# Kernel optimization log

Hardware: AMD Instinct MI355X
Metric: run time of the kernel (lower is better)

Reference implementation:

```python
import jax, jax.numpy as jnp
import numpy as np

H = 12  # num_heads

def _attn(q, k, v):
    sim = jnp.einsum('bid,bjd->bij', q, k)
    a = jax.nn.softmax(sim, axis=-1)
    return jnp.einsum('bij,bjd->bid', a, v)

def _layernorm(x, g, b, eps=1e-5):
    mu = x.mean(-1, keepdims=True)
    var = ((x - mu) ** 2).mean(-1, keepdims=True)
    return (x - mu) * jax.lax.rsqrt(var + eps) * g + b

def setup_inputs() -> dict:
    key = jax.random.key(0)
    ks = jax.random.split(key, 8)
    B, F, NP, D, DT, NT = 8, 8, 196, 768, 512, 77
    N = 1 + F * NP
    s = 0.02
    return {
        'x': jax.random.normal(ks[0], (B, N, D), jnp.float32),
        'y': jax.random.normal(ks[1], (B, NT, DT), jnp.float32),
        'y_mask': jnp.zeros((B, NT), jnp.float32),
        'f': F,
        'w_qkv': jax.random.normal(ks[2], (D, 3 * D), jnp.float32) * s,
        'w_proj': jax.random.normal(ks[3], (D, D), jnp.float32) * s,
        'b_proj': jnp.zeros((D,), jnp.float32),
        'w_kv_text': jax.random.normal(ks[4], (DT, 2 * D), jnp.float32) * s,
        'w_q_i2t': jax.random.normal(ks[5], (D, D), jnp.float32) * s,
        'w_proj_i2t': jax.random.normal(ks[6], (D, D), jnp.float32) * s,
        'b_proj_i2t': jnp.zeros((D,), jnp.float32),
        'alpha_i2t': jnp.full((1,), 0.1, jnp.float32),
        'ln_g': jnp.ones((D,), jnp.float32),
        'ln_b': jnp.zeros((D,), jnp.float32),
    }

def reference(x, y, y_mask, f, w_qkv, w_proj, b_proj, w_kv_text, w_q_i2t,
              w_proj_i2t, b_proj_i2t, alpha_i2t, ln_g, ln_b):
    B, N, D = x.shape
    d = D // H
    scale = d ** -0.5
    qkv = x @ w_qkv  # [B, N, 3D]
    q, k, v = jnp.split(qkv, 3, axis=-1)
    to_bh = lambda t: t.reshape(B, N, H, d).transpose(0, 2, 1, 3).reshape(B * H, N, d)
    q, k, v = map(to_bh, (q, k, v))
    q = q * scale
    cls_q, q_ = q[:, :1], q[:, 1:]
    cls_k, k_ = k[:, :1], k[:, 1:]
    cls_v, v_ = v[:, :1], v[:, 1:]
    # cls token attends to everything
    cls_out = _attn(cls_q, k, v)  # [B*H, 1, d]
    # divided space attention: 'b (f n) d -> (b f) n d'
    n = (N - 1) // f
    split_f = lambda t: t.reshape(B * H * f, n, d)
    q_, k_, v_ = map(split_f, (q_, k_, v_))
    rep = lambda t: jnp.broadcast_to(t[:, None], (B * H, f, 1, d)).reshape(B * H * f, 1, d)
    k_ = jnp.concatenate([rep(cls_k), k_], axis=1)  # [B*H*f, n+1, d]
    v_ = jnp.concatenate([rep(cls_v), v_], axis=1)
    out = _attn(q_, k_, v_).reshape(B * H, N - 1, d)
    out = jnp.concatenate([cls_out, out], axis=1)  # [B*H, N, d]
    out = out.reshape(B, H, N, d).transpose(0, 2, 1, 3).reshape(B, N, D)
    x_out = out @ w_proj + b_proj
    # image-to-text cross attention
    NT = y.shape[1]
    kv = (y @ w_kv_text).reshape(B, NT, 2, H, d).transpose(2, 0, 3, 1, 4)
    k_t, v_t = kv[0], kv[1]  # [B, H, NT, d]
    q_i = (_layernorm(x_out, ln_g, ln_b) @ w_q_i2t).reshape(B, N, H, d).transpose(0, 2, 1, 3)
    q_i = q_i * (d ** -0.5)
    a = jnp.einsum('bhnd,bhmd->bhnm', q_i, k_t) + y_mask[:, None, None, :]
    a = jax.nn.softmax(a, axis=-1)
    yo = jnp.einsum('bhnm,bhmd->bhnd', a, v_t).transpose(0, 2, 1, 3).reshape(B, N, D)
    yo = yo @ w_proj_i2t + b_proj_i2t
    return x_out + alpha_i2t * yo
```

## Files before the change

kernel.cpp:

```cpp
#include <hip/hip_runtime.h>

typedef __bf16 bf16x8 __attribute__((ext_vector_type(8)));
typedef float f32x4 __attribute__((ext_vector_type(4)));
typedef unsigned short us_t;

#define DEV __device__ __forceinline__

DEV float bf2f(unsigned short u) {
  union { unsigned int i; float f; } c; c.i = ((unsigned int)u) << 16; return c.f;
}
DEV unsigned short f2bf(float f) {
  union { float f; unsigned int i; } c; c.f = f;
  return (unsigned short)((c.i + 0x7FFFu + ((c.i >> 16) & 1u)) >> 16);
}
DEV unsigned int cvt_pk_bf16(float lo, float hi) {
  unsigned int r;
  asm("v_cvt_pk_bf16_f32 %0, %1, %2" : "=v"(r) : "v"(lo), "v"(hi));
  return r;
}

union FragU { bf16x8 v; unsigned short u[8]; };

DEV void gld_lds16(const void* g, void* l) {
  __builtin_amdgcn_global_load_lds((const __attribute__((address_space(1))) void*)g,
                                   (__attribute__((address_space(3))) void*)l, 16, 0, 0);
}

#define MFMA(a, b, c) __builtin_amdgcn_mfma_f32_16x16x32_bf16((a), (b), (c), 0, 0, 0)

#define BB 8
#define NN 1569
#define DD 768
#define HH 12
#define DH 64
#define FF 8
#define NFR 196
#define NTT 77
#define DT_ 512
#define MROWS 12552
#define MTEXT 616

__global__ void cvt_fused(const float* __restrict__ xin, unsigned short* __restrict__ xout, int n4x,
                          const float* __restrict__ yin, unsigned short* __restrict__ yout, int n4y) {
  int i = blockIdx.x * blockDim.x + threadIdx.x;
  int stride = gridDim.x * blockDim.x;
  int total = n4x + n4y;
  for (; i < total; i += stride) {
    const float4* src; ushort4* dst; int idx;
    if (i < n4x) { src = (const float4*)xin; dst = (ushort4*)xout; idx = i; }
    else         { src = (const float4*)yin; dst = (ushort4*)yout; idx = i - n4x; }
    float4 v = src[idx];
    ushort4 o;
    o.x = f2bf(v.x); o.y = f2bf(v.y); o.z = f2bf(v.z); o.w = f2bf(v.w);
    dst[idx] = o;
  }
}

struct TJobs {
  const float* in[5];
  unsigned short* out[5];
  int R[5], C[5];
};

__global__ __launch_bounds__(256) void transpose_all(TJobs j) {
  __shared__ float tile[32][33];
  int z = blockIdx.z;
  int R = j.R[z], C = j.C[z];
  int bx = blockIdx.x * 32;
  int by = blockIdx.y * 32;
  if (bx >= C || by >= R) return;
  const float* in = j.in[z];
  unsigned short* out = j.out[z];
  int tx = threadIdx.x & 31;
  int ty0 = threadIdx.x >> 5;
  for (int dy = 0; dy < 32; dy += 8) {
    int r = by + ty0 + dy, c = bx + tx;
    tile[ty0 + dy][tx] = (r < R && c < C) ? in[(size_t)r * C + c] : 0.f;
  }
  __syncthreads();
  for (int dy = 0; dy < 32; dy += 8) {
    int orow = bx + ty0 + dy;
    int ocol = by + tx;
    if (orow < C && ocol < R) out[(size_t)orow * R + ocol] = f2bf(tile[tx][ty0 + dy]);
  }
}

enum { EPI_QKV = 0, EPI_XOUT = 1, EPI_QI = 2, EPI_KVT = 3, EPI_FINAL = 4 };

struct EpiParams {
  float* outf;
  unsigned short *o0, *o1, *o2;
  const float *bias, *aux, *alphap;
};

template <int EPI>
__global__ __launch_bounds__(256)
void gemm_bt(const unsigned short* __restrict__ A, const unsigned short* __restrict__ Bt,
             int M, int K, EpiParams ep) {
  __shared__ __align__(16) unsigned short lA[3][128 * 32];
  __shared__ __align__(16) unsigned short lB[3][128 * 32];
  const int nbx = gridDim.x, nwg = gridDim.x * gridDim.y;
  int flat = blockIdx.y * nbx + blockIdx.x;
  {
    int q = nwg >> 3, r = nwg & 7;
    int xcd = flat & 7, i = flat >> 3;
    flat = (xcd < r ? xcd * (q + 1) : r * (q + 1) + (xcd - r) * q) + i;
  }
  const int brow = (flat / nbx) * 128, bcol = (flat % nbx) * 128;
  const int t = threadIdx.x, wave = t >> 6, lane = t & 63, g = lane >> 4, l15 = lane & 15;
  const int wr = wave >> 1, wc = wave & 1;

  int dsto[2];
  const unsigned short *pA[2], *pB[2];
#pragma unroll
  for (int c = 0; c < 2; ++c) {
    int sb = wave * 1024 + c * 512;
    int slot = sb + lane * 8;
    int row = slot >> 5;
    int gl = (slot >> 3) & 3;
    int swz = gl ^ ((row >> 1) & 3);
    int ra = brow + row; if (ra > M - 1) ra = M - 1;
    dsto[c] = sb;
    pA[c] = A + (size_t)ra * K + swz * 8;
    pB[c] = Bt + (size_t)(bcol + row) * K + swz * 8;
  }

#define STG(s, k0) do { \
    gld_lds16(pA[0] + (k0), &lA[s][dsto[0]]); \
    gld_lds16(pB[0] + (k0), &lB[s][dsto[0]]); \
    gld_lds16(pA[1] + (k0), &lA[s][dsto[1]]); \
    gld_lds16(pB[1] + (k0), &lB[s][dsto[1]]); \
    __builtin_amdgcn_sched_barrier(0); } while (0)

  f32x4 acc[4][4];
#pragma unroll
  for (int i = 0; i < 4; ++i)
#pragma unroll
    for (int j = 0; j < 4; ++j) acc[i][j] = {0.f, 0.f, 0.f, 0.f};

  const int nk = K >> 5;
  STG(0, 0);
  if (nk > 1) STG(1, 32);

  for (int kt = 0; kt < nk; ++kt) {
    const int s = kt % 3;
    if (kt + 2 < nk) STG((kt + 2) % 3, (kt + 2) << 5);
    if (kt + 2 < nk)      { asm volatile("s_waitcnt vmcnt(8)" ::: "memory"); }
    else if (kt + 1 < nk) { asm volatile("s_waitcnt vmcnt(4)" ::: "memory"); }
    else                  { asm volatile("s_waitcnt vmcnt(0)" ::: "memory"); }
    __builtin_amdgcn_sched_barrier(0);
    asm volatile("s_barrier" ::: "memory");
    __builtin_amdgcn_sched_barrier(0);

    FragU af[4], bf[4];
#pragma unroll
    for (int i = 0; i < 4; ++i) {
      int rowa = wr * 64 + i * 16 + l15;
      int swa = g ^ ((rowa >> 1) & 3);
      af[i].v = *(const bf16x8*)(&lA[s][rowa * 32 + swa * 8]);
      int rowb = wc * 64 + i * 16 + l15;
      int swb = g ^ ((rowb >> 1) & 3);
      bf[i].v = *(const bf16x8*)(&lB[s][rowb * 32 + swb * 8]);
    }
#pragma unroll
    for (int i = 0; i < 4; ++i)
#pragma unroll
      for (int j = 0; j < 4; ++j)
        acc[i][j] = MFMA(af[i].v, bf[j].v, acc[i][j]);

    asm volatile("s_waitcnt lgkmcnt(0)" ::: "memory");
    __builtin_amdgcn_sched_barrier(0);
    asm volatile("s_barrier" ::: "memory");
    __builtin_amdgcn_sched_barrier(0);
  }
#undef STG

#pragma unroll
  for (int i = 0; i < 4; ++i) {
#pragma unroll
    for (int r = 0; r < 4; ++r) {
      int mrow = brow + wr * 64 + i * 16 + g * 4 + r;
      if (mrow >= M) continue;
      int bidx = 0, nn = 0, tt = 0;
      if constexpr (EPI == EPI_QKV || EPI == EPI_QI) { bidx = mrow / NN; nn = mrow - bidx * NN; }
      if constexpr (EPI == EPI_KVT) { bidx = mrow / NTT; tt = mrow - bidx * NTT; }
#pragma unroll
      for (int j = 0; j < 4; ++j) {
        int col = bcol + wc * 64 + j * 16 + l15;
        float val = acc[i][j][r];
        if constexpr (EPI == EPI_XOUT) {
          ep.outf[(size_t)mrow * DD + col] = val + ep.bias[col];
        } else if constexpr (EPI == EPI_FINAL) {
          size_t o = (size_t)mrow * DD + col;
          ep.outf[o] = ep.aux[o] + ep.alphap[0] * (val + ep.bias[col]);
        } else if constexpr (EPI == EPI_QKV) {
          int which = col / DD; int within = col - which * DD;
          int h = within >> 6, dd2 = within & 63;
          size_t dstp = (((size_t)bidx * HH + h) * NN + nn) * DH + dd2;
          if (which == 0) ep.o0[dstp] = f2bf(val * 0.125f);
          else if (which == 1) ep.o1[dstp] = f2bf(val);
          else ep.o2[dstp] = f2bf(val);
        } else if constexpr (EPI == EPI_QI) {
          int h = col >> 6, dd2 = col & 63;
          ep.o0[(((size_t)bidx * HH + h) * NN + nn) * DH + dd2] = f2bf(val * 0.125f);
        } else if constexpr (EPI == EPI_KVT) {
          int kvi = col / DD; int within = col - kvi * DD;
          int h = within >> 6, dd2 = within & 63;
          size_t dstp = (((size_t)bidx * HH + h) * NTT + tt) * DH + dd2;
          if (kvi == 0) ep.o0[dstp] = f2bf(val);
          else ep.o1[dstp] = f2bf(val);
        }
      }
    }
  }
}

__global__ __launch_bounds__(256)
void attn_all(const unsigned short* __restrict__ qg, const unsigned short* __restrict__ kg,
              const unsigned short* __restrict__ vg, unsigned short* __restrict__ outg) {
  __shared__ __align__(16) char smem[224 * 64 * 2 + 64 * 232 * 2];
  const int t = threadIdx.x, lane = t & 63, g = lane >> 4, l15 = lane & 15;
  const int wave = t >> 6;

  if (blockIdx.x < 768) {
    unsigned short* lK = (unsigned short*)smem;
    unsigned short* lV = (unsigned short*)(smem + 224 * 64 * 2);
    const int bid = blockIdx.x, bh = bid >> 3, fi = bid & 7;
    const int b = bh / HH, h = bh - b * HH;
    const size_t base = (size_t)bh * NN * DH;

#pragma unroll
    for (int c = 0; c < 7; ++c) {
      int gI = t + 256 * c;
      int elem = gI * 8, row = elem >> 6, gl = (elem >> 3) & 7;
      int srcg = gl ^ (row & 7);
      int rr = row < 197 ? row : 196;
      int nrow = (rr == 0) ? 0 : (fi * NFR + rr);
      gld_lds16(kg + base + (size_t)nrow * DH + srcg * 8, &lK[elem]);
    }
    {
      float4 vreg[7]; int vkey[7], ve[7];
#pragma unroll
      for (int c = 0; c < 7; ++c) {
        int gI = t + 256 * c;
        if (gI < 1576) {
          int key = gI >> 3, e = gI & 7;
          int nrow = (key == 0) ? 0 : (fi * NFR + key);
          vreg[c] = *(const float4*)(vg + base + (size_t)nrow * DH + e * 8);
          vkey[c] = key; ve[c] = e;
        }
      }
#pragma unroll
      for (int c = 0; c < 7; ++c) {
        int gI = t + 256 * c;
        if (gI < 1576) {
          const unsigned short* u = (const unsigned short*)&vreg[c];
          int d0 = ve[c] * 8, key = vkey[c];
#pragma unroll
          for (int z = 0; z < 8; ++z) lV[(d0 + z) * 232 + key] = u[z];
        }
      }
      for (int idx = t; idx < 27 * 64; idx += 256) {
        int key = 197 + (idx >> 6), dd = idx & 63;
        lV[dd * 232 + key] = 0;
      }
    }
    __syncthreads();

    for (int qt = wave; qt < 13; qt += 4) {
      int qr = qt * 16 + l15; if (qr > 195) qr = 195;
      const unsigned short* qp = qg + base + (size_t)(1 + fi * NFR + qr) * DH + g * 8;
      bf16x8 bq0 = *(const bf16x8*)(qp);
      bf16x8 bq1 = *(const bf16x8*)(qp + 32);
      f32x4 s[13];
#pragma unroll
      for (int kt2 = 0; kt2 < 13; ++kt2) {
        int krow = kt2 * 16 + l15;
        int rb = krow * 64;
        int sw0 = (g ^ (krow & 7)) * 8;
        int sw1 = ((4 + g) ^ (krow & 7)) * 8;
        f32x4 a = {0.f, 0.f, 0.f, 0.f};
        a = MFMA(*(const bf16x8*)(&lK[rb + sw0]), bq0, a);
        a = MFMA(*(const bf16x8*)(&lK[rb + sw1]), bq1, a);
        s[kt2] = a;
      }
      float m = -1e30f;
#pragma unroll
      for (int kt2 = 0; kt2 < 13; ++kt2)
#pragma unroll
        for (int r = 0; r < 4; ++r) {
          int key = kt2 * 16 + g * 4 + r;
          if (key >= 197) s[kt2][r] = -1e30f;
          m = fmaxf(m, s[kt2][r]);
        }
      m = fmaxf(m, __shfl_xor(m, 16));
      m = fmaxf(m, __shfl_xor(m, 32));
      float sum = 0.f;
#pragma unroll
      for (int kt2 = 0; kt2 < 13; ++kt2)
#pragma unroll
        for (int r = 0; r < 4; ++r) { float p = __expf(s[kt2][r] - m); s[kt2][r] = p; sum += p; }
      sum += __shfl_xor(sum, 16);
      sum += __shfl_xor(sum, 32);
      float inv = 1.f / sum;
#pragma unroll
      for (int kt2 = 0; kt2 < 13; ++kt2)
#pragma unroll
        for (int r = 0; r < 4; ++r) s[kt2][r] *= inv;
      unsigned int pk2[13][2];
#pragma unroll
      for (int c2 = 0; c2 < 13; ++c2) {
        pk2[c2][0] = cvt_pk_bf16(s[c2][0], s[c2][1]);
        pk2[c2][1] = cvt_pk_bf16(s[c2][2], s[c2][3]);
      }
      f32x4 o[4];
#pragma unroll
      for (int dt = 0; dt < 4; ++dt) o[dt] = {0.f, 0.f, 0.f, 0.f};
#pragma unroll
      for (int K32 = 0; K32 < 7; ++K32) {
        FragU af;
        unsigned int* aw = (unsigned int*)&af;
#pragma unroll
        for (int w = 0; w < 4; ++w) {
          int srcl = l15 + 16 * ((((lane >> 4) & 1) * 8 + 2 * w) >> 2);
          int v0 = __shfl((int)pk2[2 * K32][w & 1], srcl, 64);
          int v1 = (2 * K32 + 1 < 13) ? __shfl((int)pk2[2 * K32 + 1][w & 1], srcl, 64) : 0;
          aw[w] = (unsigned int)((g < 2) ? v0 : v1);
        }
#pragma unroll
        for (int dt = 0; dt < 4; ++dt) {
          const bf16x8 bv = *(const bf16x8*)(&lV[(dt * 16 + l15) * 232 + K32 * 32 + g * 8]);
          o[dt] = MFMA(af.v, bv, o[dt]);
        }
      }
#pragma unroll
      for (int dt = 0; dt < 4; ++dt)
#pragma unroll
        for (int r = 0; r < 4; ++r) {
          int qrow = qt * 16 + g * 4 + r;
          if (qrow < 196) {
            size_t nrow = 1 + (size_t)fi * NFR + qrow;
            outg[((size_t)b * NN + nrow) * DD + h * DH + dt * 16 + l15] = f2bf(o[dt][r]);
          }
        }
    }
  } else {
    float* q0 = (float*)smem;
    float* sc = (float*)(smem + 256);
    float* red = (float*)(smem + 256 + NN * 4);
    float* opart2 = (float*)(smem + 256 + NN * 4 + 1024);
    const int bh = blockIdx.x - 768, b = bh / HH, h = bh - b * HH;
    const size_t base = (size_t)bh * NN * DH;
    if (t < 64) q0[t] = bf2f(qg[base + t]);
    __syncthreads();
    for (int j = t; j < NN; j += 256) {
      const unsigned short* kr = kg + base + (size_t)j * DH;
      float s = 0.f;
#pragma unroll
      for (int dd = 0; dd < 64; dd += 8) {
        float4 raw = *(const float4*)(kr + dd);
        const unsigned short* pu = (const unsigned short*)&raw;
#pragma unroll
        for (int z = 0; z < 8; ++z) s += q0[dd + z] * bf2f(pu[z]);
      }
      sc[j] = s;
    }
    __syncthreads();
    float lm = -1e30f;
    for (int j = t; j < NN; j += 256) lm = fmaxf(lm, sc[j]);
    red[t] = lm; __syncthreads();
    for (int off = 128; off > 0; off >>= 1) { if (t < off) red[t] = fmaxf(red[t], red[t + off]); __syncthreads(); }
    float m = red[0];
    __syncthreads();
    float ls = 0.f;
    for (int j = t; j < NN; j += 256) { float p = __expf(sc[j] - m); sc[j] = p; ls += p; }
    __syncthreads();
    red[t] = ls; __syncthreads();
    for (int off = 128; off > 0; off >>= 1) { if (t < off) red[t] += red[t + off]; __syncthreads(); }
    float invS = 1.f / red[0];
    int jg = t >> 3, db = t & 7;
    float o8[8];
#pragma unroll
    for (int z = 0; z < 8; ++z) o8[z] = 0.f;
    for (int j = jg; j < NN; j += 32) {
      float sj = sc[j];
      float4 raw = *(const float4*)(vg + base + (size_t)j * DH + db * 8);
      const unsigned short* pu = (const unsigned short*)&raw;
#pragma unroll
      for (int z = 0; z < 8; ++z) o8[z] += sj * bf2f(pu[z]);
    }
#pragma unroll
    for (int z = 0; z < 8; ++z) opart2[jg * 66 + db * 8 + z] = o8[z];
    __syncthreads();
    if (t < 64) {
      float r = 0.f;
      for (int p2 = 0; p2 < 32; ++p2) r += opart2[p2 * 66 + t];
      outg[((size_t)b * NN) * DD + h * DH + t] = f2bf(r * invS);
    }
  }
}

__global__ __launch_bounds__(256)
void i2t_attn(const unsigned short* __restrict__ qg, const unsigned short* __restrict__ ktg,
              const unsigned short* __restrict__ vtg, const float* __restrict__ mask,
              unsigned short* __restrict__ outg) {
  __shared__ __align__(16) unsigned short lK[80 * 64];
  __shared__ __align__(16) unsigned short lV[64 * 104];
  const int bid = blockIdx.x;
  const int bh = bid % 96, chunk = bid / 96;
  const int b = bh / HH, h = bh - b * HH;
  const int t = threadIdx.x, wave = t >> 6, lane = t & 63, g = lane >> 4, l15 = lane & 15;
  const size_t kvbase = (size_t)bh * NTT * DH;
#pragma unroll
  for (int c = 0; c < 3; ++c) {
    int gI = t + 256 * c;
    if (gI < 640) {
      int elem = gI * 8, row = elem >> 6, gl = (elem >> 3) & 7;
      int srcg = gl ^ (row & 7);
      int rr = row < NTT ? row : NTT - 1;
      gld_lds16(ktg + kvbase + (size_t)rr * DH + srcg * 8, &lK[elem]);
    }
  }
  {
    float4 vreg[3]; int vkey[3], ve[3];
#pragma unroll
    for (int c = 0; c < 3; ++c) {
      int gI = t + 256 * c;
      if (gI < 616) {
        int key = gI >> 3, e = gI & 7;
        vreg[c] = *(const float4*)(vtg + kvbase + (size_t)key * DH + e * 8);
        vkey[c] = key; ve[c] = e;
      }
    }
#pragma unroll
    for (int c = 0; c < 3; ++c) {
      int gI = t + 256 * c;
      if (gI < 616) {
        const unsigned short* u = (const unsigned short*)&vreg[c];
        int d0 = ve[c] * 8, key = vkey[c];
#pragma unroll
        for (int z = 0; z < 8; ++z) lV[(d0 + z) * 104 + key] = u[z];
      }
    }
    for (int idx = t; idx < 27 * 64; idx += 256) {
      int key = NTT + (idx >> 6), dd = idx & 63;
      lV[dd * 104 + key] = 0;
    }
  }
  __syncthreads();
  const size_t qbase = (size_t)bh * NN * DH;
#pragma unroll
  for (int i4 = 0; i4 < 4; ++i4) {
    int qt = chunk * 16 + i4 * 4 + wave;
    if (qt >= 99) continue;
    int qr = qt * 16 + l15; if (qr > NN - 1) qr = NN - 1;
    const unsigned short* qp = qg + qbase + (size_t)qr * DH + g * 8;
    bf16x8 bq0 = *(const bf16x8*)(qp);
    bf16x8 bq1 = *(const bf16x8*)(qp + 32);
    f32x4 s[5];
#pragma unroll
    for (int kt2 = 0; kt2 < 5; ++kt2) {
      int krow = kt2 * 16 + l15;
      int rb = krow * 64;
      int sw0 = (g ^ (krow & 7)) * 8;
      int sw1 = ((4 + g) ^ (krow & 7)) * 8;
      f32x4 a = {0.f, 0.f, 0.f, 0.f};
      a = MFMA(*(const bf16x8*)(&lK[rb + sw0]), bq0, a);
      a = MFMA(*(const bf16x8*)(&lK[rb + sw1]), bq1, a);
      s[kt2] = a;
    }
    float m = -1e30f;
#pragma unroll
    for (int kt2 = 0; kt2 < 5; ++kt2)
#pragma unroll
      for (int r = 0; r < 4; ++r) {
        int key = kt2 * 16 + g * 4 + r;
        if (key < NTT) s[kt2][r] += mask[b * NTT + key];
        else s[kt2][r] = -1e30f;
        m = fmaxf(m, s[kt2][r]);
      }
    m = fmaxf(m, __shfl_xor(m, 16));
    m = fmaxf(m, __shfl_xor(m, 32));
    float sum = 0.f;
#pragma unroll
    for (int kt2 = 0; kt2 < 5; ++kt2)
#pragma unroll
      for (int r = 0; r < 4; ++r) { float p = __expf(s[kt2][r] - m); s[kt2][r] = p; sum += p; }
    sum += __shfl_xor(sum, 16);
    sum += __shfl_xor(sum, 32);
    float inv = 1.f / sum;
#pragma unroll
    for (int kt2 = 0; kt2 < 5; ++kt2)
#pragma unroll
      for (int r = 0; r < 4; ++r) s[kt2][r] *= inv;
    unsigned int pk2[5][2];
#pragma unroll
    for (int c2 = 0; c2 < 5; ++c2) {
      pk2[c2][0] = cvt_pk_bf16(s[c2][0], s[c2][1]);
      pk2[c2][1] = cvt_pk_bf16(s[c2][2], s[c2][3]);
    }
    f32x4 o[4];
#pragma unroll
    for (int dt = 0; dt < 4; ++dt) o[dt] = {0.f, 0.f, 0.f, 0.f};
#pragma unroll
    for (int K32 = 0; K32 < 3; ++K32) {
      FragU af;
      unsigned int* aw = (unsigned int*)&af;
#pragma unroll
      for (int w = 0; w < 4; ++w) {
        int srcl = l15 + 16 * ((((lane >> 4) & 1) * 8 + 2 * w) >> 2);
        int v0 = __shfl((int)pk2[2 * K32][w & 1], srcl, 64);
        int v1 = (2 * K32 + 1 < 5) ? __shfl((int)pk2[2 * K32 + 1][w & 1], srcl, 64) : 0;
        aw[w] = (unsigned int)((g < 2) ? v0 : v1);
      }
#pragma unroll
      for (int dt = 0; dt < 4; ++dt) {
        const bf16x8 bv = *(const bf16x8*)(&lV[(dt * 16 + l15) * 104 + K32 * 32 + g * 8]);
        o[dt] = MFMA(af.v, bv, o[dt]);
      }
    }
#pragma unroll
    for (int dt = 0; dt < 4; ++dt)
#pragma unroll
      for (int r = 0; r < 4; ++r) {
        int qrow = qt * 16 + g * 4 + r;
        if (qrow < NN)
          outg[((size_t)b * NN + qrow) * DD + h * DH + dt * 16 + l15] = f2bf(o[dt][r]);
      }
  }
}

__global__ __launch_bounds__(256)
void ln_kernel(const float* __restrict__ x, const float* __restrict__ gam,
               const float* __restrict__ bet, unsigned short* __restrict__ out) {
  __shared__ float red[256];
  const int row = blockIdx.x, t = threadIdx.x;
  const size_t base = (size_t)row * DD;
  float v0 = x[base + t], v1 = x[base + t + 256], v2 = x[base + t + 512];
  red[t] = v0 + v1 + v2; __syncthreads();
  for (int off = 128; off > 0; off >>= 1) { if (t < off) red[t] += red[t + off]; __syncthreads(); }
  float mu = red[0] * (1.f / 768.f);
  __syncthreads();
  float d0 = v0 - mu, d1 = v1 - mu, d2 = v2 - mu;
  red[t] = d0 * d0 + d1 * d1 + d2 * d2; __syncthreads();
  for (int off = 128; off > 0; off >>= 1) { if (t < off) red[t] += red[t + off]; __syncthreads(); }
  float rs = rsqrtf(red[0] * (1.f / 768.f) + 1e-5f);
  out[base + t] = f2bf(d0 * rs * gam[t] + bet[t]);
  out[base + t + 256] = f2bf(d1 * rs * gam[t + 256] + bet[t + 256]);
  out[base + t + 512] = f2bf(d2 * rs * gam[t + 512] + bet[t + 512]);
}

static constexpr size_t SZ_WQKVT = (size_t)2304 * 768 * 2;
static constexpr size_t SZ_W768  = (size_t)768 * 768 * 2;
static constexpr size_t SZ_WKVT  = (size_t)1536 * 512 * 2;
static constexpr size_t SZ_XB    = (size_t)MROWS * DD * 2;
static constexpr size_t SZ_YB    = (size_t)MTEXT * DT_ * 2;
static constexpr size_t SZ_KT    = (size_t)96 * NTT * DH * 2;

static constexpr size_t OFF_WQKVT = 0;
static constexpr size_t OFF_WPROJT = OFF_WQKVT + SZ_WQKVT;
static constexpr size_t OFF_WKVT = OFF_WPROJT + SZ_W768;
static constexpr size_t OFF_WQIT = OFF_WKVT + SZ_WKVT;
static constexpr size_t OFF_WPIT = OFF_WQIT + SZ_W768;
static constexpr size_t OFF_XB  = OFF_WPIT + SZ_W768;
static constexpr size_t OFF_YB  = OFF_XB + SZ_XB;
static constexpr size_t OFF_QB  = OFF_YB + SZ_YB;
static constexpr size_t OFF_KB  = OFF_QB + SZ_XB;
static constexpr size_t OFF_VB  = OFF_KB + SZ_XB;
static constexpr size_t OFF_XOUT = OFF_VB + SZ_XB;

extern "C" void kernel_launch(void* const* d_in, const int* in_sizes, int n_in,
                              void* d_out, int out_size, void* d_ws, size_t ws_size,
                              hipStream_t stream) {
  const float* x      = (const float*)d_in[0];
  const float* y      = (const float*)d_in[1];
  const float* y_mask = (const float*)d_in[2];
  const float* w_qkv  = (const float*)d_in[4];
  const float* w_proj = (const float*)d_in[5];
  const float* b_proj = (const float*)d_in[6];
  const float* w_kv   = (const float*)d_in[7];
  const float* w_qi   = (const float*)d_in[8];
  const float* w_pi   = (const float*)d_in[9];
  const float* b_pi   = (const float*)d_in[10];
  const float* alpha  = (const float*)d_in[11];
  const float* ln_g   = (const float*)d_in[12];
  const float* ln_b   = (const float*)d_in[13];
  float* out = (float*)d_out;
  char* ws = (char*)d_ws;

  us_t* wqkvT = (us_t*)(ws + OFF_WQKVT);
  us_t* wprojT = (us_t*)(ws + OFF_WPROJT);
  us_t* wkvT = (us_t*)(ws + OFF_WKVT);
  us_t* wqiT = (us_t*)(ws + OFF_WQIT);
  us_t* wpiT = (us_t*)(ws + OFF_WPIT);
  us_t* xb  = (us_t*)(ws + OFF_XB);
  us_t* yb  = (us_t*)(ws + OFF_YB);
  us_t* qb  = (us_t*)(ws + OFF_QB);
  us_t* kb  = (us_t*)(ws + OFF_KB);
  us_t* vb  = (us_t*)(ws + OFF_VB);
  float* xoutf = (float*)(ws + OFF_XOUT);
  us_t* attn_out = xb;
  us_t* lnout = qb;
  us_t* qib = kb;
  us_t* ktb = vb;
  us_t* vtb = (us_t*)(ws + OFF_VB + SZ_KT);
  us_t* i2t_out = xb;

  cvt_fused<<<2048, 256, 0, stream>>>(x, xb, MROWS * DD / 4, y, yb, MTEXT * DT_ / 4);
  TJobs tj;
  tj.in[0] = w_qkv;  tj.out[0] = wqkvT;  tj.R[0] = 768; tj.C[0] = 2304;
  tj.in[1] = w_proj; tj.out[1] = wprojT; tj.R[1] = 768; tj.C[1] = 768;
  tj.in[2] = w_kv;   tj.out[2] = wkvT;   tj.R[2] = 512; tj.C[2] = 1536;
  tj.in[3] = w_qi;   tj.out[3] = wqiT;   tj.R[3] = 768; tj.C[3] = 768;
  tj.in[4] = w_pi;   tj.out[4] = wpiT;   tj.R[4] = 768; tj.C[4] = 768;
  transpose_all<<<dim3(72, 24, 5), 256, 0, stream>>>(tj);

  EpiParams e1{}; e1.o0 = qb; e1.o1 = kb; e1.o2 = vb;
  gemm_bt<EPI_QKV><<<dim3(18, 99), 256, 0, stream>>>(xb, wqkvT, MROWS, 768, e1);

  attn_all<<<864, 256, 0, stream>>>(qb, kb, vb, attn_out);

  EpiParams e2{}; e2.outf = xoutf; e2.bias = b_proj;
  gemm_bt<EPI_XOUT><<<dim3(6, 99), 256, 0, stream>>>(attn_out, wprojT, MROWS, 768, e2);

  ln_kernel<<<MROWS, 256, 0, stream>>>(xoutf, ln_g, ln_b, lnout);

  EpiParams e3{}; e3.o0 = qib;
  gemm_bt<EPI_QI><<<dim3(6, 99), 256, 0, stream>>>(lnout, wqiT, MROWS, 768, e3);

  EpiParams e4{}; e4.o0 = ktb; e4.o1 = vtb;
  gemm_bt<EPI_KVT><<<dim3(12, 5), 256, 0, stream>>>(yb, wkvT, MTEXT, 512, e4);

  i2t_attn<<<dim3(96 * 7), 256, 0, stream>>>(qib, ktb, vtb, y_mask, i2t_out);

  EpiParams e5{}; e5.outf = out; e5.bias = b_pi; e5.aux = xoutf; e5.alphap = alpha;
  gemm_bt<EPI_FINAL><<<dim3(6, 99), 256, 0, stream>>>(i2t_out, wpiT, MROWS, 768, e5);
}
```

Baseline: 332.9 us.

## Use BK=64 double-buffered LDS with XOR swizzle in bf16 GEMM

Changes the GEMM main loop from a triple-buffered K-tile of 32 to a double-buffered K-tile of 64, with a new byte-level XOR swizzle for the LDS layout. Each iteration now issues twice as many loads and MFMAs per barrier pair, which halves the number of synchronisation points and amortises their overhead. The trade-off is less prefetch depth (one stage ahead instead of two) and higher LDS usage (64KB vs 48KB), which may reduce occupancy or expose more memory latency.

```diff
diff --git a/kernel.cpp b/kernel.cpp
--- a/kernel.cpp
+++ b/kernel.cpp
@@ -97,8 +97,8 @@
 __global__ __launch_bounds__(256)
 void gemm_bt(const unsigned short* __restrict__ A, const unsigned short* __restrict__ Bt,
              int M, int K, EpiParams ep) {
-  __shared__ __align__(16) unsigned short lA[3][128 * 32];
-  __shared__ __align__(16) unsigned short lB[3][128 * 32];
+  __shared__ __align__(16) unsigned short lA[2][128 * 64];
+  __shared__ __align__(16) unsigned short lB[2][128 * 64];
   const int nbx = gridDim.x, nwg = gridDim.x * gridDim.y;
   int flat = blockIdx.y * nbx + blockIdx.x;
   {
@@ -110,70 +110,84 @@
   const int t = threadIdx.x, wave = t >> 6, lane = t & 63, g = lane >> 4, l15 = lane & 15;
   const int wr = wave >> 1, wc = wave & 1;
 
-  int dsto[2];
-  const unsigned short *pA[2], *pB[2];
-#pragma unroll
-  for (int c = 0; c < 2; ++c) {
-    int sb = wave * 1024 + c * 512;
-    int slot = sb + lane * 8;
-    int row = slot >> 5;
-    int gl = (slot >> 3) & 3;
-    int swz = gl ^ ((row >> 1) & 3);
-    int ra = brow + row; if (ra > M - 1) ra = M - 1;
-    dsto[c] = sb;
-    pA[c] = A + (size_t)ra * K + swz * 8;
-    pB[c] = Bt + (size_t)(bcol + row) * K + swz * 8;
-  }
-
-#define STG(s, k0) do { \
-    gld_lds16(pA[0] + (k0), &lA[s][dsto[0]]); \
-    gld_lds16(pB[0] + (k0), &lB[s][dsto[0]]); \
-    gld_lds16(pA[1] + (k0), &lA[s][dsto[1]]); \
-    gld_lds16(pB[1] + (k0), &lB[s][dsto[1]]); \
+  int dsto[4];
+  const unsigned short *pA[4], *pB[4];
+#pragma unroll
+  for (int j = 0; j < 4; ++j) {
+    int p = wave * 4096 + j * 1024 + lane * 16;
+    int q = p ^ (((p >> 7) & 7) << 4);
+    int r = q >> 7;
+    int e = (q & 127) >> 1;
+    dsto[j] = (wave * 4096 + j * 1024) >> 1;
+    int ra = brow + r; if (ra > M - 1) ra = M - 1;
+    pA[j] = A + (size_t)ra * K + e;
+    pB[j] = Bt + (size_t)(bcol + r) * K + e;
+  }
+
+#define STG(bufi, k0) do { \
+    gld_lds16(pA[0] + (k0), &lA[bufi][dsto[0]]); \
+    gld_lds16(pB[0] + (k0), &lB[bufi][dsto[0]]); \
+    gld_lds16(pA[1] + (k0), &lA[bufi][dsto[1]]); \
+    gld_lds16(pB[1] + (k0), &lB[bufi][dsto[1]]); \
+    gld_lds16(pA[2] + (k0), &lA[bufi][dsto[2]]); \
+    gld_lds16(pB[2] + (k0), &lB[bufi][dsto[2]]); \
+    gld_lds16(pA[3] + (k0), &lA[bufi][dsto[3]]); \
+    gld_lds16(pB[3] + (k0), &lB[bufi][dsto[3]]); \
     __builtin_amdgcn_sched_barrier(0); } while (0)
 
+#define SWZ(lb) ((lb) ^ ((((lb) >> 7) & 7) << 4))
+
   f32x4 acc[4][4];
 #pragma unroll
   for (int i = 0; i < 4; ++i)
 #pragma unroll
     for (int j = 0; j < 4; ++j) acc[i][j] = {0.f, 0.f, 0.f, 0.f};
 
-  const int nk = K >> 5;
+  const int nk = K >> 6;
   STG(0, 0);
-  if (nk > 1) STG(1, 32);
-
+  int buf = 0;
   for (int kt = 0; kt < nk; ++kt) {
-    const int s = kt % 3;
-    if (kt + 2 < nk) STG((kt + 2) % 3, (kt + 2) << 5);
-    if (kt + 2 < nk)      { asm volatile("s_waitcnt vmcnt(8)" ::: "memory"); }
-    else if (kt + 1 < nk) { asm volatile("s_waitcnt vmcnt(4)" ::: "memory"); }
-    else                  { asm volatile("s_waitcnt vmcnt(0)" ::: "memory"); }
+    if (kt + 1 < nk) {
+      STG(buf ^ 1, (kt + 1) << 6);
+      asm volatile("s_waitcnt vmcnt(8)" ::: "memory");
+    } else {
+      asm volatile("s_waitcnt vmcnt(0)" ::: "memory");
+    }
     __builtin_amdgcn_sched_barrier(0);
     asm volatile("s_barrier" ::: "memory");
     __builtin_amdgcn_sched_barrier(0);
 
-    FragU af[4], bf[4];
+    const char* bA = (const char*)&lA[buf][0];
+    const char* bB = (const char*)&lB[buf][0];
+    FragU af[4][2], bf[4][2];
 #pragma unroll
     for (int i = 0; i < 4; ++i) {
       int rowa = wr * 64 + i * 16 + l15;
-      int swa = g ^ ((rowa >> 1) & 3);
-      af[i].v = *(const bf16x8*)(&lA[s][rowa * 32 + swa * 8]);
       int rowb = wc * 64 + i * 16 + l15;
-      int swb = g ^ ((rowb >> 1) & 3);
-      bf[i].v = *(const bf16x8*)(&lB[s][rowb * 32 + swb * 8]);
+#pragma unroll
+      for (int kk = 0; kk < 2; ++kk) {
+        int lba = rowa * 128 + kk * 64 + g * 16;
+        int lbb = rowb * 128 + kk * 64 + g * 16;
+        af[i][kk].v = *(const bf16x8*)(bA + SWZ(lba));
+        bf[i][kk].v = *(const bf16x8*)(bB + SWZ(lbb));
+      }
     }
 #pragma unroll
     for (int i = 0; i < 4; ++i)
 #pragma unroll
       for (int j = 0; j < 4; ++j)
-        acc[i][j] = MFMA(af[i].v, bf[j].v, acc[i][j]);
+#pragma unroll
+        for (int kk = 0; kk < 2; ++kk)
+          acc[i][j] = MFMA(af[i][kk].v, bf[j][kk].v, acc[i][j]);
 
     asm volatile("s_waitcnt lgkmcnt(0)" ::: "memory");
     __builtin_amdgcn_sched_barrier(0);
     asm volatile("s_barrier" ::: "memory");
     __builtin_amdgcn_sched_barrier(0);
+    buf ^= 1;
   }
 #undef STG
+#undef SWZ
 
 #pragma unroll
   for (int i = 0; i < 4; ++i) {
```

Result: slower. 385.3 us (+15.7%).
